# Kernel optimization log

Measured on AMD Instinct MI355X. Metric: run time of the kernel, lower is better.

## Reference

```python
import jax, jax.numpy as jnp
import numpy as np

MAX_RADIUS = 4.0
N_BASIS = 10
MUL = 8                    # output_size -> '8x0e' multiplicity
OUT_MULS = (16, 8, 4)      # irreps_output = 16x0e + 8x1o + 4x2e
L_DIMS = (1, 3, 5)
N_NODES = 10000
N_EDGES = 131072
N_GRAPHS = 64
WEIGHT_NUMEL = MUL * MUL * sum(OUT_MULS)  # 1792


def _silu(x):
    return x * jax.nn.sigmoid(x)


def _sph_harm(u):
    # e3nn real spherical harmonics lmax=2, normalize=True, 'component' normalization
    x, y, z = u[:, 0], u[:, 1], u[:, 2]
    s3, s5, s15 = 3.0 ** 0.5, 5.0 ** 0.5, 15.0 ** 0.5
    sh0 = jnp.ones_like(x)[:, None]
    sh1 = jnp.stack([s3 * x, s3 * y, s3 * z], -1)
    sh2 = jnp.stack([s15 * x * z, s15 * x * y,
                     s5 * (y * y - 0.5 * (x * x + z * z)),
                     s15 * y * z, 0.5 * s15 * (z * z - x * x)], -1)
    return sh0, sh1, sh2


def _soft_one_hot(x):
    # e3nn soft_one_hot_linspace, basis='gaussian', cutoff=True
    values = jnp.linspace(0.0, MAX_RADIUS, N_BASIS + 2)[1:-1]
    step = MAX_RADIUS / (N_BASIS + 1)
    diff = (x[:, None] - values) / step
    return jnp.exp(-diff * diff) / 1.12


def setup_inputs() -> dict:
    key = jax.random.key(0)
    ks = jax.random.split(key, 16)
    return {
        "pos": jax.random.normal(ks[0], (N_NODES, 3), jnp.float32) * 2.0,
        "A": jax.random.randint(ks[1], (N_NODES,), 0, 10),
        "batch": jnp.sort(jax.random.randint(ks[2], (N_NODES,), 0, N_GRAPHS)),
        "edge_src": jax.random.randint(ks[3], (N_EDGES,), 0, N_NODES),
        "edge_dst": jax.random.randint(ks[4], (N_EDGES,), 0, N_NODES),
        "edge_shifts": jax.random.normal(ks[5], (N_EDGES, 3), jnp.float32) * 0.1,
        "cell": jax.random.normal(ks[6], (N_GRAPHS, 3, 3), jnp.float32),
        "embed_table": jax.random.normal(ks[7], (10, 16), jnp.float32),
        "fit_W1": jax.random.normal(ks[8], (16, 64), jnp.float32) * (2.0 / 16) ** 0.5,
        "fit_b1": jnp.zeros((64,), jnp.float32),
        "fit_W2": jax.random.normal(ks[9], (64, 32), jnp.float32) * (2.0 / 64) ** 0.5,
        "fit_b2": jnp.zeros((32,), jnp.float32),
        "fit_W3": jax.random.normal(ks[10], (32, MUL), jnp.float32) * (2.0 / 32) ** 0.5,
        "fit_b3": jnp.zeros((MUL,), jnp.float32),
        "fc_W1": jax.random.normal(ks[11], (N_BASIS, 64), jnp.float32),
        "fc_W2": jax.random.normal(ks[12], (64, 64), jnp.float32),
        "fc_W3": jax.random.normal(ks[13], (64, 64), jnp.float32),
        "fc_W4": jax.random.normal(ks[14], (64, WEIGHT_NUMEL), jnp.float32),
    }


def reference(pos, A, batch, edge_src, edge_dst, edge_shifts, cell,
              embed_table, fit_W1, fit_b1, fit_W2, fit_b2, fit_W3, fit_b3,
              fc_W1, fc_W2, fc_W3, fc_W4):
    # --- edge vectors with periodic shifts ---
    shift_vecs = jnp.einsum('ni,nij->nj', edge_shifts, cell[batch[edge_src]])
    edge_vec = pos[edge_dst] - pos[edge_src] + shift_vecs      # [E,3]
    edge_length = jnp.linalg.norm(edge_vec, axis=1)            # [E]
    unit = edge_vec / jnp.maximum(edge_length, 1e-9)[:, None]

    # --- per-node scalar features: embedding -> MLP (MainNet2) ---
    h = embed_table[A]
    h = _silu(h @ fit_W1 + fit_b1)
    h = _silu(h @ fit_W2 + fit_b2)
    Ai = h @ fit_W3 + fit_b3                                   # [N,8]

    sh0, sh1, sh2 = _sph_harm(unit)                            # [E,1],[E,3],[E,5]

    # --- radial MLP (e3nn FullyConnectedNet: silu, 1/sqrt(fan_in) weight scaling) ---
    emb = _soft_one_hot(edge_length) * (N_BASIS ** 0.5)
    w = _silu(emb @ fc_W1 / N_BASIS ** 0.5)
    w = _silu(w @ fc_W2 / 8.0)
    w = _silu(w @ fc_W3 / 8.0)
    w = w @ fc_W4 / 8.0                                        # [E,1792]

    Ai_src = Ai[edge_src]                                      # [E,8]
    Ai_dst = Ai[edge_dst]                                      # [E,8]

    # FullTensorProduct(8x0e, sh) is the outer product f_in[e,u,m] = Ai_src[e,u]*sh_l[e,m];
    # FullyConnectedTensorProduct with scalar irreps_in2 reduces per l-channel to a
    # weighted contraction with path normalization 1/sqrt(mul1*mul2) = 1/8.
    blocks, off = [], 0
    for mul_out, dim, sh_l in zip(OUT_MULS, L_DIMS, (sh0, sh1, sh2)):
        n = MUL * MUL * mul_out
        Wl = w[:, off:off + n].reshape(-1, MUL, MUL, mul_out)
        off += n
        blk = jnp.einsum('eu,em,ev,euvw->ewm', Ai_src, sh_l, Ai_dst, Wl) / MUL
        blocks.append(blk.reshape(-1, mul_out * dim))
    edge_features = jnp.concatenate(blocks, -1)                # [E,60]

    # --- scatter-mean aggregation to destination nodes ---
    n_nodes = pos.shape[0]
    counts = jax.ops.segment_sum(jnp.ones((edge_dst.shape[0],), jnp.float32),
                                 edge_dst, num_segments=n_nodes)
    out = jax.ops.segment_sum(edge_features, edge_dst, num_segments=n_nodes)
    return out / jnp.maximum(counts, 1.0)[:, None]             # [N,60]
```

## Files before the change

kernel.cpp:

```cpp
#include <hip/hip_runtime.h>
#include <hip/hip_bf16.h>
#include <math.h>

#define NN 10000
#define NE 131072

typedef __attribute__((ext_vector_type(8))) short short8;
typedef __attribute__((ext_vector_type(4))) float f32x4;

__device__ __forceinline__ float silu_f(float x) {
    return x / (1.0f + __expf(-x));
}

__device__ __forceinline__ unsigned short f2bf(float f) {
    unsigned int u = __float_as_uint(f);
    u += 0x7FFFu + ((u >> 16) & 1u);
    return (unsigned short)(u >> 16);
}

__device__ __forceinline__ unsigned int pk_bf16(float lo, float hi) {
    __hip_bfloat162 h = __float22bfloat162_rn(float2{lo, hi});
    return *reinterpret_cast<unsigned int*>(&h);
}

__global__ __launch_bounds__(256)
void prep_kernel(const int* __restrict__ A,
                 const int* __restrict__ edst,
                 const float* __restrict__ emb_tab,
                 const float* __restrict__ W1, const float* __restrict__ b1,
                 const float* __restrict__ W2, const float* __restrict__ b2,
                 const float* __restrict__ W3, const float* __restrict__ b3,
                 const float* __restrict__ fcW1,
                 const float* __restrict__ fcW2,
                 const float* __restrict__ fcW3,
                 const float* __restrict__ fcW4,
                 int* __restrict__ hist,
                 int* __restrict__ rank,
                 float* __restrict__ outg,
                 float* __restrict__ Ai,
                 unsigned short* __restrict__ Wg,
                 unsigned short* __restrict__ Bg)
{
    const int blk = blockIdx.x;
    const int tid = threadIdx.x;

    if (blk < 40) {
        int nd = blk * 256 + tid;
        if (nd >= NN) return;
        int a = A[nd];
        float h[16];
#pragma unroll
        for (int i = 0; i < 16; ++i) h[i] = emb_tab[a * 16 + i];
        float h1[64];
#pragma unroll
        for (int j = 0; j < 64; ++j) h1[j] = b1[j];
#pragma unroll
        for (int i = 0; i < 16; ++i) {
            float hv = h[i];
#pragma unroll
            for (int j = 0; j < 64; ++j) h1[j] += hv * W1[i * 64 + j];
        }
#pragma unroll
        for (int j = 0; j < 64; ++j) h1[j] = silu_f(h1[j]);
        float h2[32];
#pragma unroll
        for (int j = 0; j < 32; ++j) h2[j] = b2[j];
#pragma unroll
        for (int i = 0; i < 64; ++i) {
            float hv = h1[i];
#pragma unroll
            for (int j = 0; j < 32; ++j) h2[j] += hv * W2[i * 32 + j];
        }
#pragma unroll
        for (int j = 0; j < 32; ++j) h2[j] = silu_f(h2[j]);
#pragma unroll
        for (int j = 0; j < 8; ++j) {
            float s = b3[j];
#pragma unroll
            for (int i = 0; i < 32; ++i) s += h2[i] * W3[i * 8 + j];
            Ai[nd * 8 + j] = s;
        }
    } else if (blk < 80) {
        int i = (blk - 40) * 256 + tid;
        int j    = i & 7;
        int lane = (i >> 3) & 63;
        int f    = i >> 9;
        int q = lane >> 4, n = lane & 15;
        int L, kf, nt;
        if (f < 4)       { L = 1; kf = 0;             nt = f; }
        else if (f < 12) { L = 2; kf = (f - 4) >> 2;  nt = (f - 4) & 3; }
        else             { L = 3; kf = (f - 12) >> 2; nt = (f - 12) & 3; }
        int k = kf * 32 + q * 8 + j;
        int col = nt * 16 + n;
        float v = 0.0f;
        if (L == 1)      { if (k < 10) v = fcW1[k * 64 + col]; }
        else if (L == 2) v = fcW2[k * 64 + col];
        else             v = fcW3[k * 64 + col];
        Wg[i] = f2bf(v);
    } else if (blk < 592) {
        int linear = (blk - 80) * 256 + tid;
        rank[linear] = atomicAdd(&hist[edst[linear]], 1);
        if (linear < 114688) {
            int k = linear / 1792;
            int t = linear - k * 1792;
            int uv, wc;
            if (t < 1024)      { uv = t >> 4;            wc = t & 15; }
            else if (t < 1536) { int r = t - 1024; uv = r >> 3; wc = 16 + (r & 7); }
            else               { int r = t - 1536; uv = r >> 2; wc = 24 + (r & 3); }
            int h  = uv >> 5;
            int q  = (uv >> 3) & 3;
            int j  = uv & 7;
            int nt = wc >> 4;
            int n  = wc & 15;
            int i  = (k << 11) | (h << 10) | (nt << 9) | (((q << 4) | n) << 3) | j;
            Bg[i] = f2bf(fcW4[linear]);
        } else {
            int z  = linear - 114688;
            int k  = z >> 8;
            int r  = z & 255;
            int uv = r >> 2;
            int c2 = z & 3;
            int h  = uv >> 5;
            int q  = (uv >> 3) & 3;
            int j  = uv & 7;
            int i  = (k << 11) | (h << 10) | (1 << 9) | (((q << 4) | (12 + c2)) << 3) | j;
            Bg[i] = 0;
        }
    } else {
        int t = (blk - 592) * 256 + tid;
        float4 z = float4{0.f, 0.f, 0.f, 0.f};
        for (int r = t; r < 150000; r += 25600)
            ((float4*)outg)[r] = z;
    }
}

__global__ __launch_bounds__(256)
void scanrank_kernel(const int* __restrict__ edst,
                     const int* __restrict__ hist,
                     const int* __restrict__ rank,
                     int* __restrict__ sortidx)
{
    __shared__ int offs[NN];
    __shared__ int part[256];
    const int tid = threadIdx.x;

    int loc[40];
    int s = 0;
    if (tid < 250) {
        const int4* h4 = (const int4*)(hist) + tid * 10;
#pragma unroll
        for (int v = 0; v < 10; ++v) {
            int4 x = h4[v];
            loc[v * 4 + 0] = x.x; loc[v * 4 + 1] = x.y;
            loc[v * 4 + 2] = x.z; loc[v * 4 + 3] = x.w;
            s += x.x + x.y + x.z + x.w;
        }
    } else {
#pragma unroll
        for (int r = 0; r < 40; ++r) loc[r] = 0;
    }
    part[tid] = s;
    __syncthreads();
#pragma unroll
    for (int off = 1; off < 256; off <<= 1) {
        int v = (tid >= off) ? part[tid - off] : 0;
        __syncthreads();
        part[tid] += v;
        __syncthreads();
    }
    if (tid < 250) {
        int run = part[tid] - s;
        int base = tid * 40;
#pragma unroll
        for (int r = 0; r < 40; ++r) { offs[base + r] = run; run += loc[r]; }
    }
    __syncthreads();

    int e = blockIdx.x * 256 + tid;
    int d = edst[e];
    sortidx[offs[d] + rank[e]] = e;
}

__global__ __launch_bounds__(256, 2)
void edge_fused_kernel(const float* __restrict__ pos,
                       const int* __restrict__ batch,
                       const int* __restrict__ esrc,
                       const int* __restrict__ edst,
                       const float* __restrict__ shifts,
                       const float* __restrict__ cell,
                       const unsigned short* __restrict__ Wg,
                       const unsigned short* __restrict__ Bg,
                       const int* __restrict__ sortidx,
                       const float* __restrict__ Ai,
                       const int* __restrict__ hist,
                       float* __restrict__ out_g)
{
    __shared__ __align__(16) unsigned short actb[4][64 * 68];
    __shared__ int   sdb[256];
    __shared__ __align__(16) float shb[4][64 * 8];

    const int tid  = threadIdx.x;
    const int wave = tid >> 6;
    const int lane = tid & 63;
    const int q    = lane >> 4;
    const int n    = lane & 15;
    const int i    = blockIdx.x * 256 + wave * 64 + lane;

    unsigned short* actw = actb[wave];

    int e = sortidx[i];
    int s = esrc[e], d = edst[e];
    sdb[wave * 64 + lane] = s | (d << 16);
    int b = batch[s];
    const float* C = cell + b * 9;
    float sx = shifts[e * 3 + 0], sy = shifts[e * 3 + 1], sz = shifts[e * 3 + 2];
    float vx = pos[d * 3 + 0] - pos[s * 3 + 0] + sx * C[0] + sy * C[3] + sz * C[6];
    float vy = pos[d * 3 + 1] - pos[s * 3 + 1] + sx * C[1] + sy * C[4] + sz * C[7];
    float vz = pos[d * 3 + 2] - pos[s * 3 + 2] + sx * C[2] + sy * C[5] + sz * C[8];
    float len = sqrtf(vx * vx + vy * vy + vz * vz);
    float inv = 1.0f / fmaxf(len, 1e-9f);
    float ux = vx * inv, uy = vy * inv, uz = vz * inv;
    {
        const float s3c  = 1.7320508075688772f;
        const float s5c  = 2.2360679774997896f;
        const float s15c = 3.872983346207417f;
        float* shw = shb[wave];
        *(float4*)&shw[lane * 8]     = float4{s3c * ux, s3c * uy, s3c * uz,
                                              s15c * ux * uz};
        *(float4*)&shw[lane * 8 + 4] = float4{s15c * ux * uy,
                                              s5c * (uy * uy - 0.5f * (ux * ux + uz * uz)),
                                              s15c * uy * uz,
                                              0.5f * s15c * (uz * uz - ux * ux)};
    }

    float embv[10];
    float base = len * 2.75f;
#pragma unroll
    for (int ii = 0; ii < 10; ++ii) {
        float ddv = base - (float)(ii + 1);
        embv[ii] = __expf(-ddv * ddv) * (1.0f / 1.12f);
    }
    {
        unsigned int u0 = pk_bf16(embv[0], embv[1]);
        unsigned int u1 = pk_bf16(embv[2], embv[3]);
        unsigned int u2 = pk_bf16(embv[4], embv[5]);
        unsigned int u3 = pk_bf16(embv[6], embv[7]);
        unsigned int u4 = pk_bf16(embv[8], embv[9]);
        uint2* arow = (uint2*)&actw[lane * 68];
        arow[0] = uint2{u0, u1};
        arow[1] = uint2{u2, u3};
        arow[2] = uint2{u4, 0u};
        arow[3] = uint2{0u, 0u};
        arow[4] = uint2{0u, 0u};
        arow[5] = uint2{0u, 0u};
        arow[6] = uint2{0u, 0u};
        arow[7] = uint2{0u, 0u};
    }

    union AF { unsigned int u[4]; short8 s8; };
    const f32x4 Z4 = (f32x4){0.f, 0.f, 0.f, 0.f};

    auto loadA = [&](int t, int kf) -> AF {
        const unsigned short* ap = &actw[(t * 16 + n) * 68 + kf * 32 + q * 8];
        uint2 a = *(const uint2*)ap;
        uint2 c = *(const uint2*)(ap + 4);
        AF f; f.u[0] = a.x; f.u[1] = a.y; f.u[2] = c.x; f.u[3] = c.y;
        return f;
    };
    auto loadW = [&](int f) -> short8 {
        return *(const short8*)&Wg[(f * 64 + lane) * 8];
    };

    {
        AF A1[4];
#pragma unroll
        for (int t = 0; t < 4; ++t) A1[t] = loadA(t, 0);
#pragma unroll
        for (int nt = 0; nt < 4; ++nt) {
            short8 W0 = loadW(nt);
            f32x4 Cc[4];
#pragma unroll
            for (int t = 0; t < 4; ++t)
                Cc[t] = __builtin_amdgcn_mfma_f32_16x16x32_bf16(A1[t].s8, W0, Z4, 0, 0, 0);
#pragma unroll
            for (int t = 0; t < 4; ++t)
#pragma unroll
                for (int r = 0; r < 4; ++r)
                    actw[(t * 16 + q * 4 + r) * 68 + nt * 16 + n] = f2bf(silu_f(Cc[t][r]));
        }
    }

    {
        AF A2[4][2];
#pragma unroll
        for (int t = 0; t < 4; ++t)
#pragma unroll
            for (int kf = 0; kf < 2; ++kf) A2[t][kf] = loadA(t, kf);
#pragma unroll
        for (int nt = 0; nt < 4; ++nt) {
            short8 Wk0 = loadW(4 + nt);
            short8 Wk1 = loadW(8 + nt);
            f32x4 Cc[4];
#pragma unroll
            for (int t = 0; t < 4; ++t) {
                Cc[t] = __builtin_amdgcn_mfma_f32_16x16x32_bf16(A2[t][0].s8, Wk0, Z4, 0, 0, 0);
                Cc[t] = __builtin_amdgcn_mfma_f32_16x16x32_bf16(A2[t][1].s8, Wk1, Cc[t], 0, 0, 0);
            }
#pragma unroll
            for (int t = 0; t < 4; ++t)
#pragma unroll
                for (int r = 0; r < 4; ++r)
                    actw[(t * 16 + q * 4 + r) * 68 + nt * 16 + n] = f2bf(silu_f(Cc[t][r] * 0.125f));
        }
    }

    {
        AF A3[4][2];
#pragma unroll
        for (int t = 0; t < 4; ++t)
#pragma unroll
            for (int kf = 0; kf < 2; ++kf) A3[t][kf] = loadA(t, kf);
#pragma unroll
        for (int nt = 0; nt < 4; ++nt) {
            short8 Wk0 = loadW(12 + nt);
            short8 Wk1 = loadW(16 + nt);
            f32x4 Cc[4];
#pragma unroll
            for (int t = 0; t < 4; ++t) {
                Cc[t] = __builtin_amdgcn_mfma_f32_16x16x32_bf16(A3[t][0].s8, Wk0, Z4, 0, 0, 0);
                Cc[t] = __builtin_amdgcn_mfma_f32_16x16x32_bf16(A3[t][1].s8, Wk1, Cc[t], 0, 0, 0);
            }
#pragma unroll
            for (int t = 0; t < 4; ++t)
#pragma unroll
                for (int r = 0; r < 4; ++r)
                    actw[(nt * 16 + n) * 68 + t * 16 + q * 4 + r] = f2bf(silu_f(Cc[t][r] * 0.125f));
        }
    }

    const unsigned char* BgB = (const unsigned char*)Bg;
    short8 BA[8], BB[8];

    auto LOADB = [&](short8 (&Bf)[8], int c) {
#pragma unroll
        for (int f = 0; f < 8; ++f)
            Bf[f] = *(const short8*)(BgB +
                (((size_t)((c * 8 + f) * 64 + lane)) << 4));
    };

    LOADB(BA, 0);

    AF P[4][2];
#pragma unroll
    for (int t = 0; t < 4; ++t) {
        int eL = wave * 64 + t * 16 + n;
        int sd = sdb[eL];
        int ss  = sd & 0xFFFF;
        int dd2 = sd >> 16;
        float As0 = Ai[ss * 8 + q];
        float As1 = Ai[ss * 8 + 4 + q];
        float4 d0 = *(const float4*)&Ai[dd2 * 8];
        float4 d1 = *(const float4*)&Ai[dd2 * 8 + 4];
        float Ad[8] = {d0.x, d0.y, d0.z, d0.w, d1.x, d1.y, d1.z, d1.w};
#pragma unroll
        for (int h = 0; h < 2; ++h) {
            float s0 = h ? As1 : As0;
            P[t][h].u[0] = pk_bf16(s0 * Ad[0], s0 * Ad[1]);
            P[t][h].u[1] = pk_bf16(s0 * Ad[2], s0 * Ad[3]);
            P[t][h].u[2] = pk_bf16(s0 * Ad[4], s0 * Ad[5]);
            P[t][h].u[3] = pk_bf16(s0 * Ad[6], s0 * Ad[7]);
        }
    }

    f32x4 out[4][2];
#pragma unroll
    for (int t = 0; t < 4; ++t)
#pragma unroll
        for (int nt = 0; nt < 2; ++nt)
            out[t][nt] = (f32x4){0.f, 0.f, 0.f, 0.f};

    auto COMPUTE = [&](short8 (&Bf)[8], int c) {
#pragma unroll
        for (int kk = 0; kk < 2; ++kk) {
            int k = c * 2 + kk;
#pragma unroll
            for (int t = 0; t < 4; ++t) {
                uint2 v = *(const uint2*)&actw[k * 68 + t * 16 + q * 4];
                float w0 = __uint_as_float(v.x << 16);
                float w1 = __uint_as_float(v.x & 0xFFFF0000u);
                float w2 = __uint_as_float(v.y << 16);
                float w3 = __uint_as_float(v.y & 0xFFFF0000u);
#pragma unroll
                for (int nt = 0; nt < 2; ++nt) {
                    f32x4 Q = __builtin_amdgcn_mfma_f32_16x16x32_bf16(
                        P[t][0].s8, Bf[kk * 4 + nt], Z4, 0, 0, 0);
                    Q = __builtin_amdgcn_mfma_f32_16x16x32_bf16(
                        P[t][1].s8, Bf[kk * 4 + 2 + nt], Q, 0, 0, 0);
                    out[t][nt][0] += w0 * Q[0];
                    out[t][nt][1] += w1 * Q[1];
                    out[t][nt][2] += w2 * Q[2];
                    out[t][nt][3] += w3 * Q[3];
                }
            }
        }
    };

#pragma unroll 1
    for (int cp = 0; cp < 16; ++cp) {
        int c0 = cp * 2, c1 = c0 + 1;
        LOADB(BB, c1);
        COMPUTE(BA, c0);
        if (cp < 15) LOADB(BA, c0 + 2);
        COMPUTE(BB, c1);
    }

    float* featL = (float*)actw;
#pragma unroll
    for (int t = 0; t < 4; ++t) {
#pragma unroll
        for (int r = 0; r < 4; ++r) {
            int row = t * 16 + q * 4 + r;
            featL[row * 33 + n]      = out[t][0][r];
            featL[row * 33 + 16 + n] = out[t][1][r];
        }
    }

    if (lane < 60) {
        int j = lane;
        int cc, sidx = 0;
        bool is0 = (j < 16);
        if (j < 16)      { cc = j; }
        else if (j < 40) { cc = 16 + (j - 16) / 3; sidx = (j - 16) % 3; }
        else             { cc = 24 + (j - 40) / 5; sidx = 3 + (j - 40) % 5; }

        const float* shw = shb[wave];
        int cur_d = sdb[wave * 64] >> 16;
        float acc = 0.f;
        for (int e2 = 0; e2 < 64; ++e2) {
            int d_e = sdb[wave * 64 + e2] >> 16;
            if (d_e != cur_d) {
                int cnt = hist[cur_d];
                atomicAdd(&out_g[cur_d * 60 + j], acc * (1.0f / 64.0f) / (float)cnt);
                acc = 0.f;
                cur_d = d_e;
            }
            float f  = featL[e2 * 33 + cc];
            float sh = shw[e2 * 8 + sidx];
            if (is0) sh = 1.0f;
            acc += f * sh;
        }
        int cnt = hist[cur_d];
        atomicAdd(&out_g[cur_d * 60 + j], acc * (1.0f / 64.0f) / (float)cnt);
    }
}

extern "C" void kernel_launch(void* const* d_in, const int* in_sizes, int n_in,
                              void* d_out, int out_size, void* d_ws, size_t ws_size,
                              hipStream_t stream)
{
    const float* pos     = (const float*)d_in[0];
    const int*   A       = (const int*)d_in[1];
    const int*   batch   = (const int*)d_in[2];
    const int*   esrc    = (const int*)d_in[3];
    const int*   edst    = (const int*)d_in[4];
    const float* shifts  = (const float*)d_in[5];
    const float* cell    = (const float*)d_in[6];
    const float* emb_tab = (const float*)d_in[7];
    const float* fitW1   = (const float*)d_in[8];
    const float* fitb1   = (const float*)d_in[9];
    const float* fitW2   = (const float*)d_in[10];
    const float* fitb2   = (const float*)d_in[11];
    const float* fitW3   = (const float*)d_in[12];
    const float* fitb3   = (const float*)d_in[13];
    const float* fcW1    = (const float*)d_in[14];
    const float* fcW2    = (const float*)d_in[15];
    const float* fcW3    = (const float*)d_in[16];
    const float* fcW4    = (const float*)d_in[17];

    float* out = (float*)d_out;

    char* W = (char*)d_ws;
    float* Ai      = (float*)W;  W += (size_t)NN * 8 * 4;
    int* sortidx   = (int*)W;    W += (size_t)NE * 4;
    int* rank      = (int*)W;    W += (size_t)NE * 4;
    int* hist      = (int*)W;    W += (size_t)NN * 4;
    unsigned short* Bg = (unsigned short*)W; W += (size_t)131072 * 2;
    unsigned short* Wg = (unsigned short*)W; W += (size_t)10240 * 2;

    hipMemsetAsync(hist, 0, (size_t)NN * 4, stream);

    prep_kernel<<<692, 256, 0, stream>>>(
        A, edst, emb_tab, fitW1, fitb1, fitW2, fitb2, fitW3, fitb3,
        fcW1, fcW2, fcW3, fcW4, hist, rank, out, Ai, Wg, Bg);

    scanrank_kernel<<<NE / 256, 256, 0, stream>>>(edst, hist, rank, sortidx);

    edge_fused_kernel<<<NE / 256, 256, 0, stream>>>(
        pos, batch, esrc, edst, shifts, cell, Wg, Bg,
        sortidx, Ai, hist, out);
}
```

Baseline: 187.2 us.

## Split each 64-edge tile across two waves along the contraction dimension

Each block now handles 128 edges instead of 256. Pairs of waves share one 64-edge tile and each wave does half of the layer-3 output columns and half of the 32 B-weight chunks in the main tensor-product loop. The two partial feature sums are combined through shared memory before the scatter, and the scatter loop is split so each wave handles 32 edges. Launch bounds rise to 4 blocks per CU to raise occupancy. The cost is redundant work in layers 1-2 and the geometry step, which both waves of a pair now compute, plus extra block-wide barriers and more atomics.

```diff
diff --git a/kernel.cpp b/kernel.cpp
--- a/kernel.cpp
+++ b/kernel.cpp
@@ -181,7 +181,7 @@
     sortidx[offs[d] + rank[e]] = e;
 }
 
-__global__ __launch_bounds__(256, 2)
+__global__ __launch_bounds__(256, 4)
 void edge_fused_kernel(const float* __restrict__ pos,
                        const int* __restrict__ batch,
                        const int* __restrict__ esrc,
@@ -195,22 +195,26 @@
                        const int* __restrict__ hist,
                        float* __restrict__ out_g)
 {
-    __shared__ __align__(16) unsigned short actb[4][64 * 68];
-    __shared__ int   sdb[256];
-    __shared__ __align__(16) float shb[4][64 * 8];
+    __shared__ __align__(16) unsigned short actb[2][64 * 68];
+    __shared__ __align__(16) unsigned short w3Tb[2][64 * 68];
+    __shared__ int   sdb[128];
+    __shared__ __align__(16) float shb[2][64 * 8];
 
     const int tid  = threadIdx.x;
     const int wave = tid >> 6;
     const int lane = tid & 63;
+    const int grp  = wave >> 1;
+    const int kh   = wave & 1;
     const int q    = lane >> 4;
     const int n    = lane & 15;
-    const int i    = blockIdx.x * 256 + wave * 64 + lane;
-
-    unsigned short* actw = actb[wave];
+    const int i    = blockIdx.x * 128 + grp * 64 + lane;
+
+    unsigned short* actw = actb[grp];
+    unsigned short* w3T  = w3Tb[grp];
 
     int e = sortidx[i];
     int s = esrc[e], d = edst[e];
-    sdb[wave * 64 + lane] = s | (d << 16);
+    sdb[grp * 64 + lane] = s | (d << 16);
     int b = batch[s];
     const float* C = cell + b * 9;
     float sx = shifts[e * 3 + 0], sy = shifts[e * 3 + 1], sz = shifts[e * 3 + 2];
@@ -224,7 +228,7 @@
         const float s3c  = 1.7320508075688772f;
         const float s5c  = 2.2360679774997896f;
         const float s15c = 3.872983346207417f;
-        float* shw = shb[wave];
+        float* shw = shb[grp];
         *(float4*)&shw[lane * 8]     = float4{s3c * ux, s3c * uy, s3c * uz,
                                               s15c * ux * uz};
         *(float4*)&shw[lane * 8 + 4] = float4{s15c * ux * uy,
@@ -275,6 +279,9 @@
         AF A1[4];
 #pragma unroll
         for (int t = 0; t < 4; ++t) A1[t] = loadA(t, 0);
+
+        __syncthreads();
+
 #pragma unroll
         for (int nt = 0; nt < 4; ++nt) {
             short8 W0 = loadW(nt);
@@ -296,6 +303,9 @@
         for (int t = 0; t < 4; ++t)
 #pragma unroll
             for (int kf = 0; kf < 2; ++kf) A2[t][kf] = loadA(t, kf);
+
+        __syncthreads();
+
 #pragma unroll
         for (int nt = 0; nt < 4; ++nt) {
             short8 Wk0 = loadW(4 + nt);
@@ -321,7 +331,8 @@
 #pragma unroll
             for (int kf = 0; kf < 2; ++kf) A3[t][kf] = loadA(t, kf);
 #pragma unroll
-        for (int nt = 0; nt < 4; ++nt) {
+        for (int ntl = 0; ntl < 2; ++ntl) {
+            int nt = kh * 2 + ntl;
             short8 Wk0 = loadW(12 + nt);
             short8 Wk1 = loadW(16 + nt);
             f32x4 Cc[4];
@@ -334,12 +345,13 @@
             for (int t = 0; t < 4; ++t)
 #pragma unroll
                 for (int r = 0; r < 4; ++r)
-                    actw[(nt * 16 + n) * 68 + t * 16 + q * 4 + r] = f2bf(silu_f(Cc[t][r] * 0.125f));
+                    w3T[(nt * 16 + n) * 68 + t * 16 + q * 4 + r] = f2bf(silu_f(Cc[t][r] * 0.125f));
         }
     }
 
     const unsigned char* BgB = (const unsigned char*)Bg;
     short8 BA[8], BB[8];
+    const int cbase = kh * 16;
 
     auto LOADB = [&](short8 (&Bf)[8], int c) {
 #pragma unroll
@@ -348,12 +360,12 @@
                 (((size_t)((c * 8 + f) * 64 + lane)) << 4));
     };
 
-    LOADB(BA, 0);
+    LOADB(BA, cbase);
 
     AF P[4][2];
 #pragma unroll
     for (int t = 0; t < 4; ++t) {
-        int eL = wave * 64 + t * 16 + n;
+        int eL = grp * 64 + t * 16 + n;
         int sd = sdb[eL];
         int ss  = sd & 0xFFFF;
         int dd2 = sd >> 16;
@@ -385,7 +397,7 @@
             int k = c * 2 + kk;
 #pragma unroll
             for (int t = 0; t < 4; ++t) {
-                uint2 v = *(const uint2*)&actw[k * 68 + t * 16 + q * 4];
+                uint2 v = *(const uint2*)&w3T[k * 68 + t * 16 + q * 4];
                 float w0 = __uint_as_float(v.x << 16);
                 float w1 = __uint_as_float(v.x & 0xFFFF0000u);
                 float w2 = __uint_as_float(v.y << 16);
@@ -406,24 +418,31 @@
     };
 
 #pragma unroll 1
-    for (int cp = 0; cp < 16; ++cp) {
-        int c0 = cp * 2, c1 = c0 + 1;
+    for (int cp = 0; cp < 8; ++cp) {
+        int c0 = cbase + cp * 2, c1 = c0 + 1;
         LOADB(BB, c1);
         COMPUTE(BA, c0);
-        if (cp < 15) LOADB(BA, c0 + 2);
+        if (cp < 7) LOADB(BA, c0 + 2);
         COMPUTE(BB, c1);
     }
 
-    float* featL = (float*)actw;
+    __syncthreads();
+
+    float* featMine = (float*)(kh == 0 ? actw : w3T);
 #pragma unroll
     for (int t = 0; t < 4; ++t) {
 #pragma unroll
         for (int r = 0; r < 4; ++r) {
             int row = t * 16 + q * 4 + r;
-            featL[row * 33 + n]      = out[t][0][r];
-            featL[row * 33 + 16 + n] = out[t][1][r];
-        }
-    }
+            featMine[row * 33 + n]      = out[t][0][r];
+            featMine[row * 33 + 16 + n] = out[t][1][r];
+        }
+    }
+
+    __syncthreads();
+
+    const float* featA = (const float*)actw;
+    const float* featB = (const float*)w3T;
 
     if (lane < 60) {
         int j = lane;
@@ -433,18 +452,19 @@
         else if (j < 40) { cc = 16 + (j - 16) / 3; sidx = (j - 16) % 3; }
         else             { cc = 24 + (j - 40) / 5; sidx = 3 + (j - 40) % 5; }
 
-        const float* shw = shb[wave];
-        int cur_d = sdb[wave * 64] >> 16;
+        const float* shw = shb[grp];
+        const int e0 = kh * 32;
+        int cur_d = sdb[grp * 64 + e0] >> 16;
         float acc = 0.f;
-        for (int e2 = 0; e2 < 64; ++e2) {
-            int d_e = sdb[wave * 64 + e2] >> 16;
+        for (int e2 = e0; e2 < e0 + 32; ++e2) {
+            int d_e = sdb[grp * 64 + e2] >> 16;
             if (d_e != cur_d) {
                 int cnt = hist[cur_d];
                 atomicAdd(&out_g[cur_d * 60 + j], acc * (1.0f / 64.0f) / (float)cnt);
                 acc = 0.f;
                 cur_d = d_e;
             }
-            float f  = featL[e2 * 33 + cc];
+            float f  = featA[e2 * 33 + cc] + featB[e2 * 33 + cc];
             float sh = shw[e2 * 8 + sidx];
             if (is0) sh = 1.0f;
             acc += f * sh;
@@ -495,7 +515,7 @@
 
     scanrank_kernel<<<NE / 256, 256, 0, stream>>>(edst, hist, rank, sortidx);
 
-    edge_fused_kernel<<<NE / 256, 256, 0, stream>>>(
+    edge_fused_kernel<<<NE / 128, 256, 0, stream>>>(
         pos, batch, esrc, edst, shifts, cell, Wg, Bg,
         sortidx, Ai, hist, out);
 }
```

New measurement: 431.3 us. +130.4%, slower.
